# Optimization experiments

Measured on AMD Instinct MI355X. Metric: run time of the kernel, lower is better.

## Reference

```python
import jax, jax.numpy as jnp
import numpy as np

B, S, D = 8, 2048, 768
SCALE = jnp.sqrt(jnp.float32(D))


def setup_inputs() -> dict:
    key = jax.random.key(0)
    ks = jax.random.split(key, 9)
    sd = 1.0 / np.sqrt(D)
    return {
        "x": jax.random.normal(ks[0], (B, S, D), jnp.float32),
        "Wq": jax.random.normal(ks[1], (D, D), jnp.float32) * sd,
        "bq": jax.random.normal(ks[2], (D,), jnp.float32) * sd,
        "Wk": jax.random.normal(ks[3], (D, D), jnp.float32) * sd,
        "bk": jax.random.normal(ks[4], (D,), jnp.float32) * sd,
        "Wv": jax.random.normal(ks[5], (D, D), jnp.float32) * sd,
        "bv": jax.random.normal(ks[6], (D,), jnp.float32) * sd,
        "Wp": jax.random.normal(ks[7], (D, D), jnp.float32) * sd,
        "bp": jax.random.normal(ks[8], (D,), jnp.float32) * sd,
    }


def reference(x, Wq, bq, Wk, bk, Wv, bv, Wp, bp):
    # Linear layers: y = x @ W^T + b (torch nn.Linear convention)
    Q = jnp.einsum("bsd,ed->bse", x, Wq) + bq
    K = jnp.einsum("bsd,ed->bse", x, Wk) + bk
    V = jnp.einsum("bsd,ed->bse", x, Wv) + bv
    # Full attention matrix (no head split in original module)
    alpha = jnp.einsum("bqd,bkd->bqk", Q, K) / SCALE  # [B,S,S]
    alpha = jax.nn.softmax(alpha, axis=-1)
    # dropout is identity in eval mode
    out = jnp.einsum("bqk,bkd->bqd", alpha, V)
    out = jnp.einsum("bsd,ed->bse", out, Wp) + bp
    return out
```

## Files before the change

### kernel.cpp

```cpp
#include <hip/hip_runtime.h>
#include <stdint.h>


typedef __attribute__((ext_vector_type(8))) short short8;
typedef __attribute__((ext_vector_type(4))) float f32x4;

typedef const __attribute__((address_space(1))) void gvoid_t;
typedef __attribute__((address_space(3))) void lvoid_t;

__device__ __forceinline__ float b2f(unsigned short u) {
  union { unsigned int u; float f; } v;
  v.u = ((unsigned int)u) << 16;
  return v.f;
}
__device__ __forceinline__ unsigned short f2b(float f) {
  union { float f; unsigned int u; } v; v.f = f;
  unsigned int u = v.u;
  return (unsigned short)((u + 0x7fffu + ((u >> 16) & 1u)) >> 16);
}

struct Cvt9 {
  const void* s[9];
  unsigned short* d[9];
  long long n8[9];
  long long total8;
};

__global__ __launch_bounds__(256) void convert_inputs(Cvt9 C) {
  long long g = (long long)blockIdx.x * 256 + threadIdx.x;
  if (g >= C.total8) return;
  int s = 0;
  long long off = g;
  while (off >= C.n8[s]) { off -= C.n8[s]; ++s; }
  const float* sf = (const float*)C.s[s] + off * 8;
  unsigned short* dp = C.d[s] + off * 8;
  float4 a = ((const float4*)sf)[0];
  float4 b = ((const float4*)sf)[1];
  uint4 o;
  o.x = (unsigned int)f2b(a.x) | ((unsigned int)f2b(a.y) << 16);
  o.y = (unsigned int)f2b(a.z) | ((unsigned int)f2b(a.w) << 16);
  o.z = (unsigned int)f2b(b.x) | ((unsigned int)f2b(b.y) << 16);
  o.w = (unsigned int)f2b(b.z) | ((unsigned int)f2b(b.w) << 16);
  *(uint4*)dp = o;
}

__device__ __forceinline__ void gemm256(
    const unsigned short* __restrict__ Ag,
    const unsigned short* __restrict__ Bg,
    const int lda, const int ldb, const int NT,
    unsigned short* lds, f32x4 (&acc)[8][4])
{
  const int t    = threadIdx.x;
  const int w    = t >> 6;
  const int lane = t & 63;
  const int lo   = lane & 15;
  const int quad = lane >> 4;
  const int wr   = w >> 2;
  const int wcn  = w & 3;
  const int swz  = ((t & 7) ^ ((t >> 3) & 7)) << 3;
  const int wslot = w * 512;

  const unsigned lbase = (unsigned)(uintptr_t)(void*)lds;
  const unsigned sb0 = (unsigned)((quad ^ (lo & 7)) << 4);
  const unsigned sb1 = (unsigned)(((4 + quad) ^ (lo & 7)) << 4);
  const unsigned aA0 = lbase + wr * 16384 + lo * 128 + sb0;
  const unsigned aA1 = lbase + wr * 16384 + lo * 128 + sb1;
  const unsigned aB0 = lbase + 32768 + (wcn >> 1) * 16384 + ((wcn & 1) * 64 + lo) * 128 + sb0;
  const unsigned aB1 = lbase + 32768 + (wcn >> 1) * 16384 + ((wcn & 1) * 64 + lo) * 128 + sb1;

  short8 af[4][2], bf0[2][2], bf1[2][2];

#define STG(gb, ld, kt, q, reg)                                                   \
  __builtin_amdgcn_global_load_lds(                                               \
      (gvoid_t*)((gb) + (size_t)((q) * 64 + (t >> 3)) * (ld) + (kt) * 64 + swz),  \
      (lvoid_t*)((reg) + wslot), 16, 0, 0)
#define SA02(kt) { unsigned short* r_ = lds + ((kt) & 1) * 32768;         \
                   STG(Ag, lda, (kt), 0, r_); STG(Ag, lda, (kt), 2, r_ + 8192); }
#define SA13(kt) { unsigned short* r_ = lds + ((kt) & 1) * 32768;         \
                   STG(Ag, lda, (kt), 1, r_ + 4096); STG(Ag, lda, (kt), 3, r_ + 12288); }
#define SB01(kt) { unsigned short* r_ = lds + ((kt) & 1) * 32768 + 16384; \
                   STG(Bg, ldb, (kt), 0, r_); STG(Bg, ldb, (kt), 1, r_ + 4096); }
#define SB23(kt) { unsigned short* r_ = lds + ((kt) & 1) * 32768 + 16384; \
                   STG(Bg, ldb, (kt), 2, r_ + 8192); STG(Bg, ldb, (kt), 3, r_ + 12288); }
#define DSR(d, a, IMM) asm volatile("ds_read_b128 %0, %1 offset:" #IMM : "=v"(d) : "v"(a))
#define RDA(MH, bo) {                                                 \
  const unsigned a0_ = aA0 + (bo) + (MH) * 8192;                      \
  const unsigned a1_ = aA1 + (bo) + (MH) * 8192;                      \
  DSR(af[0][0], a0_, 0);    DSR(af[0][1], a1_, 0);                    \
  DSR(af[1][0], a0_, 2048); DSR(af[1][1], a1_, 2048);                 \
  DSR(af[2][0], a0_, 4096); DSR(af[2][1], a1_, 4096);                 \
  DSR(af[3][0], a0_, 6144); DSR(af[3][1], a1_, 6144); }
#define RDB(BF, NH, bo) {                                             \
  const unsigned b0_ = aB0 + (bo) + (NH) * 4096;                      \
  const unsigned b1_ = aB1 + (bo) + (NH) * 4096;                      \
  DSR(BF[0][0], b0_, 0);    DSR(BF[0][1], b1_, 0);                    \
  DSR(BF[1][0], b0_, 2048); DSR(BF[1][1], b1_, 2048); }
#define MMA(MH, NH, BF) {                                                     \
  __builtin_amdgcn_s_barrier();                                               \
  asm volatile("s_waitcnt lgkmcnt(0)" ::: "memory");                          \
  __builtin_amdgcn_sched_barrier(0);                                          \
  __builtin_amdgcn_s_setprio(1);                                              \
  _Pragma("unroll") for (int kc = 0; kc < 2; ++kc)                            \
  _Pragma("unroll") for (int mi = 0; mi < 4; ++mi)                            \
  _Pragma("unroll") for (int ni = 0; ni < 2; ++ni)                            \
    acc[(MH)*4 + mi][(NH)*2 + ni] = __builtin_amdgcn_mfma_f32_16x16x32_bf16(  \
        af[mi][kc], BF[ni][kc], acc[(MH)*4 + mi][(NH)*2 + ni], 0, 0, 0);      \
  __builtin_amdgcn_s_setprio(0);                                              \
  __builtin_amdgcn_sched_barrier(0);                                          \
  __builtin_amdgcn_s_barrier(); }
#define VM(n) asm volatile("s_waitcnt vmcnt(" #n ")" ::: "memory")

  SA02(0); SB01(0); SB23(0); SA13(0);
  SA02(1); SB01(1); SB23(1); SA13(1);
  VM(8);
  __builtin_amdgcn_s_barrier();

  for (int kt = 0; kt < NT - 2; ++kt) {
    const unsigned bo = (unsigned)(kt & 1) << 16;
    RDA(0, bo); RDB(bf0, 0, bo);                          MMA(0, 0, bf0);
    RDB(bf1, 1, bo); SA02(kt + 2);                        MMA(0, 1, bf1);
    RDA(1, bo); SB01(kt + 2); SB23(kt + 2);               MMA(1, 0, bf0);
    SA13(kt + 2); VM(8);                                  MMA(1, 1, bf1);
  }
  {
    const unsigned bo = (unsigned)(NT & 1) << 16;
    RDA(0, bo); RDB(bf0, 0, bo);                          MMA(0, 0, bf0);
    RDB(bf1, 1, bo);                                      MMA(0, 1, bf1);
    RDA(1, bo);                                           MMA(1, 0, bf0);
    VM(0);                                                MMA(1, 1, bf1);
  }
  {
    const unsigned bo = (unsigned)((NT - 1) & 1) << 16;
    RDA(0, bo); RDB(bf0, 0, bo);                          MMA(0, 0, bf0);
    RDB(bf1, 1, bo);                                      MMA(0, 1, bf1);
    RDA(1, bo);                                           MMA(1, 0, bf0);
                                                          MMA(1, 1, bf1);
  }
#undef STG
#undef SA02
#undef SA13
#undef SB01
#undef SB23
#undef DSR
#undef RDA
#undef RDB
#undef MMA
#undef VM
}

template<int MODE>
__device__ __forceinline__ void epi_bf16(
    unsigned short* Ls, f32x4 (&acc)[8][4], int h,
    const unsigned short* bias_n0, const float* rlbase, float scale,
    unsigned short* Cg, int ldc)
{
  const int t = threadIdx.x, w = t >> 6, lane = t & 63;
  const int lo = lane & 15, quad = lane >> 4, wr = w >> 2, wcn = w & 3;
  __syncthreads();
  if (wr == h) {
    float bvv[4];
    if (MODE == 0) {
#pragma unroll
      for (int nf = 0; nf < 4; ++nf) bvv[nf] = b2f(bias_n0[wcn * 64 + nf * 16 + lo]);
    }
#pragma unroll
    for (int mf = 0; mf < 8; ++mf) {
      const int r0 = mf * 16 + quad * 4;
      float rv[4];
      if (MODE == 3) {
#pragma unroll
        for (int r = 0; r < 4; ++r) rv[r] = __builtin_amdgcn_rcpf(rlbase[h * 128 + r0 + r]);
      }
#pragma unroll
      for (int nf = 0; nf < 4; ++nf) {
        const int col = wcn * 64 + nf * 16 + lo;
#pragma unroll
        for (int r = 0; r < 4; ++r) {
          float v = acc[mf][nf][r];
          if (MODE == 0)      v += bvv[nf];
          else if (MODE == 2) v = __expf(fminf(v * scale, 30.f));
          else if (MODE == 3) v *= rv[r];
          Ls[(r0 + r) * 264 + col] = f2b(v);
        }
      }
    }
  }
  __syncthreads();
#pragma unroll
  for (int u0 = 0; u0 < 8; ++u0) {
    const int u = u0 * 512 + t, row = u >> 5, c16 = (u & 31) * 8;
    *(uint4*)(Cg + (size_t)(h * 128 + row) * ldc + c16) = *(const uint4*)(Ls + row * 264 + c16);
  }
}

__global__ __launch_bounds__(512, 2) void qkv_k(
    const unsigned short* __restrict__ xb,
    const unsigned short* __restrict__ Wq, const unsigned short* __restrict__ bq,
    const unsigned short* __restrict__ Wk, const unsigned short* __restrict__ bk,
    const unsigned short* __restrict__ Wv, const unsigned short* __restrict__ bv,
    unsigned short* __restrict__ qb, unsigned short* __restrict__ kb,
    unsigned short* __restrict__ vt)
{
  __shared__ unsigned short smem[65536];
  const int sel = blockIdx.y / 3;
  const int n0  = (blockIdx.y % 3) * 256;
  const int m0  = blockIdx.x * 256;

  const unsigned short* W;
  const unsigned short* bi;
  if (sel == 0)      { W = Wq; bi = bq; }
  else if (sel == 1) { W = Wk; bi = bk; }
  else               { W = Wv; bi = bv; }

  f32x4 acc[8][4] = {};
  gemm256(xb + (size_t)m0 * 768, W + (size_t)n0 * 768, 768, 768, 12, smem, acc);

  if (sel < 2) {
    unsigned short* dst = (sel == 0 ? qb : kb) + (size_t)m0 * 768 + n0;
    epi_bf16<0>(smem, acc, 0, bi + n0, nullptr, 0.f, dst, 768);
    epi_bf16<0>(smem, acc, 1, bi + n0, nullptr, 0.f, dst, 768);
    return;
  }

  const int t = threadIdx.x, w = t >> 6, lane = t & 63;
  const int lo = lane & 15, quad = lane >> 4, wr = w >> 2, wcn = w & 3;
  const int bb2 = m0 >> 11, sin = m0 & 2047;
  unsigned short* Ls = smem;
#pragma unroll
  for (int eh = 0; eh < 2; ++eh) {
    __syncthreads();
    if ((wcn >> 1) == eh) {
#pragma unroll
      for (int mf = 0; mf < 8; ++mf) {
        const int row = wr * 128 + mf * 16 + quad * 4;
#pragma unroll
        for (int nf = 0; nf < 4; ++nf) {
          const int colL = (wcn & 1) * 64 + nf * 16 + lo;
          const float bvv = b2f(bi[n0 + eh * 128 + colL]);
          ushort4 pk;
          pk.x = f2b(acc[mf][nf][0] + bvv);
          pk.y = f2b(acc[mf][nf][1] + bvv);
          pk.z = f2b(acc[mf][nf][2] + bvv);
          pk.w = f2b(acc[mf][nf][3] + bvv);
          *(ushort4*)(Ls + colL * 264 + row) = pk;
        }
      }
    }
    __syncthreads();
    unsigned short* Vb = vt + (size_t)bb2 * 1572864 + (size_t)(n0 + eh * 128) * 2048 + sin;
#pragma unroll
    for (int u0 = 0; u0 < 8; ++u0) {
      const int u = u0 * 512 + t, e = u >> 5, s16 = (u & 31) * 8;
      *(uint4*)(Vb + (size_t)e * 2048 + s16) = *(const uint4*)(Ls + e * 264 + s16);
    }
  }
}

__global__ __launch_bounds__(512, 2) void score_k(
    const unsigned short* __restrict__ Q, const unsigned short* __restrict__ Kb,
    unsigned short* __restrict__ E, float* __restrict__ rl, float scale)
{
  __shared__ unsigned short smem[65536];
  const int m0 = blockIdx.x * 256, n0 = blockIdx.y * 256, bz = blockIdx.z;

  f32x4 acc[8][4] = {};
  gemm256(Q + (size_t)bz * 1572864 + (size_t)m0 * 768,
          Kb + (size_t)bz * 1572864 + (size_t)n0 * 768, 768, 768, 12, smem, acc);

  const int t = threadIdx.x;
  unsigned short* Eg = E + (size_t)bz * 4194304 + (size_t)m0 * 2048 + n0;
#pragma unroll
  for (int h = 0; h < 2; ++h) {
    epi_bf16<2>(smem, acc, h, nullptr, nullptr, scale, Eg, 2048);
    const int row = t >> 2, seg = t & 3;
    const unsigned short* lr = smem + row * 264 + seg * 64;
    float s = 0.f;
#pragma unroll
    for (int q8 = 0; q8 < 8; ++q8) {
      const int qq = ((q8 + row) & 7) * 8;
      uint4 v = *(const uint4*)(lr + qq);
      unsigned int uu[4] = {v.x, v.y, v.z, v.w};
#pragma unroll
      for (int c = 0; c < 4; ++c)
        s += b2f((unsigned short)(uu[c] & 0xffffu)) + b2f((unsigned short)(uu[c] >> 16));
    }
    s += __shfl_xor(s, 1);
    s += __shfl_xor(s, 2);
    if (seg == 0) atomicAdd(rl + bz * 2048 + m0 + h * 128 + row, s);
  }
}

__global__ __launch_bounds__(512, 2) void pv_k(
    const unsigned short* __restrict__ E, const unsigned short* __restrict__ Vt,
    const float* __restrict__ rl, unsigned short* __restrict__ attn)
{
  __shared__ unsigned short smem[65536];
  const int m0 = blockIdx.x * 256, n0 = blockIdx.y * 256, bz = blockIdx.z;

  f32x4 acc[8][4] = {};
  gemm256(E + (size_t)bz * 4194304 + (size_t)m0 * 2048,
          Vt + (size_t)bz * 1572864 + (size_t)n0 * 2048, 2048, 2048, 32, smem, acc);

  const float* rlb = rl + bz * 2048 + m0;
  unsigned short* Cg = attn + (size_t)bz * 1572864 + (size_t)m0 * 768 + n0;
  epi_bf16<3>(smem, acc, 0, nullptr, rlb, 0.f, Cg, 768);
  epi_bf16<3>(smem, acc, 1, nullptr, rlb, 0.f, Cg, 768);
}

__global__ __launch_bounds__(512, 2) void out_k(
    const unsigned short* __restrict__ attn,
    const unsigned short* __restrict__ Wp, const unsigned short* __restrict__ bp,
    float* __restrict__ Of)
{
  __shared__ unsigned short smem[65536];
  const int m0 = blockIdx.x * 256, n0 = blockIdx.y * 256;

  f32x4 acc[8][4] = {};
  gemm256(attn + (size_t)m0 * 768, Wp + (size_t)n0 * 768, 768, 768, 12, smem, acc);

  const int t = threadIdx.x, w = t >> 6, lane = t & 63;
  const int lo = lane & 15, quad = lane >> 4, wr = w >> 2, wcn = w & 3;
  float* Lf = (float*)smem;
#pragma unroll
  for (int p = 0; p < 4; ++p) {
    __syncthreads();
    if (wr == (p >> 1)) {
#pragma unroll
      for (int mi = 0; mi < 4; ++mi) {
        const int mf = (p & 1) * 4 + mi;
        const int r0 = mi * 16 + quad * 4;
#pragma unroll
        for (int nf = 0; nf < 4; ++nf) {
          const int col = wcn * 64 + nf * 16 + lo;
          const float bvv = b2f(bp[n0 + col]);
#pragma unroll
          for (int r = 0; r < 4; ++r)
            Lf[(r0 + r) * 264 + col] = acc[mf][nf][r] + bvv;
        }
      }
    }
    __syncthreads();
#pragma unroll
    for (int u0 = 0; u0 < 8; ++u0) {
      const int u = u0 * 512 + t, row = u >> 6, c4 = (u & 63) * 4;
      *(float4*)(Of + (size_t)(m0 + p * 64 + row) * 768 + n0 + c4) =
          *(const float4*)(Lf + row * 264 + c4);
    }
  }
}

extern "C" void kernel_launch(void* const* d_in, const int* in_sizes, int n_in,
                              void* d_out, int out_size, void* d_ws, size_t ws_size,
                              hipStream_t stream) {
  (void)in_sizes; (void)n_in; (void)out_size; (void)ws_size;

  char* ws = (char*)d_ws;
  float* rl    = (float*)(ws + 4096);
  unsigned short* wcv = (unsigned short*)(ws + ((size_t)1 << 20));
  unsigned short* qb  = (unsigned short*)(ws + ((size_t)8  << 20));
  unsigned short* kb  = (unsigned short*)(ws + ((size_t)32 << 20));
  unsigned short* vt  = (unsigned short*)(ws + ((size_t)56 << 20));
  unsigned short* eb  = (unsigned short*)(ws + ((size_t)80 << 20));
  unsigned short* xb  = eb;
  unsigned short* attn = qb;

  unsigned short* wqb = wcv;
  unsigned short* bqb = wcv + 589824;
  unsigned short* wkb = wcv + 590592;
  unsigned short* bkb = wcv + 1180416;
  unsigned short* wvb = wcv + 1181184;
  unsigned short* bvb = wcv + 1771008;
  unsigned short* wpb = wcv + 1771776;
  unsigned short* bpb = wcv + 2361600;

  const float inv_scale = 0.036084391824351615f;

  Cvt9 cv;
  cv.s[0] = d_in[0]; cv.d[0] = xb;  cv.n8[0] = 12582912 / 8;
  cv.s[1] = d_in[1]; cv.d[1] = wqb; cv.n8[1] = 589824 / 8;
  cv.s[2] = d_in[2]; cv.d[2] = bqb; cv.n8[2] = 768 / 8;
  cv.s[3] = d_in[3]; cv.d[3] = wkb; cv.n8[3] = 589824 / 8;
  cv.s[4] = d_in[4]; cv.d[4] = bkb; cv.n8[4] = 768 / 8;
  cv.s[5] = d_in[5]; cv.d[5] = wvb; cv.n8[5] = 589824 / 8;
  cv.s[6] = d_in[6]; cv.d[6] = bvb; cv.n8[6] = 768 / 8;
  cv.s[7] = d_in[7]; cv.d[7] = wpb; cv.n8[7] = 589824 / 8;
  cv.s[8] = d_in[8]; cv.d[8] = bpb; cv.n8[8] = 768 / 8;
  cv.total8 = (12582912 + 4 * (589824 + 768)) / 8;
  convert_inputs<<<(unsigned)((cv.total8 + 255) / 256), dim3(256), 0, stream>>>(cv);

  hipMemsetAsync(rl, 0, 16384 * sizeof(float), stream);

  qkv_k<<<dim3(64, 9, 1), dim3(512), 0, stream>>>(xb, wqb, bqb, wkb, bkb, wvb, bvb, qb, kb, vt);

  score_k<<<dim3(8, 8, 8), dim3(512), 0, stream>>>(qb, kb, eb, rl, inv_scale);

  pv_k<<<dim3(8, 3, 8), dim3(512), 0, stream>>>(eb, vt, rl, attn);

  out_k<<<dim3(64, 3, 1), dim3(512), 0, stream>>>(attn, wpb, bpb, (float*)d_out);
}
```

Before: 353.8 us.

## Use 256x192 GEMM tiles for the N=768 kernels to improve CU occupancy

Templates the 256x256 bf16 MFMA GEMM core on the number of N fragments per wave, so the qkv, pv and out kernels can use 256x192 tiles while score_k keeps 256x256. With N=768 split into four tiles instead of three, the grids grow (e.g. pv from 192 to 256 blocks), which is meant to fill the MI355X CUs better and reduce tail imbalance. LDS footprint, B staging, wait counts and epilogues are adjusted for the narrower tile. The cost is lower per-tile arithmetic intensity and more A-tile reloads.

```diff
diff --git a/kernel.cpp b/kernel.cpp
--- a/kernel.cpp
+++ b/kernel.cpp
@@ -44,11 +44,12 @@
   *(uint4*)dp = o;
 }
 
+template<int NQ>
 __device__ __forceinline__ void gemm256(
     const unsigned short* __restrict__ Ag,
     const unsigned short* __restrict__ Bg,
     const int lda, const int ldb, const int NT,
-    unsigned short* lds, f32x4 (&acc)[8][4])
+    unsigned short* lds, f32x4 (&acc)[8][NQ])
 {
   const int t    = threadIdx.x;
   const int w    = t >> 6;
@@ -59,14 +60,17 @@
   const int wcn  = w & 3;
   const int swz  = ((t & 7) ^ ((t >> 3) & 7)) << 3;
   const int wslot = w * 512;
+  constexpr int SBUF_B = (4 + NQ) * 8192;
+  constexpr int SBUF_S = SBUF_B / 2;
 
   const unsigned lbase = (unsigned)(uintptr_t)(void*)lds;
   const unsigned sb0 = (unsigned)((quad ^ (lo & 7)) << 4);
   const unsigned sb1 = (unsigned)(((4 + quad) ^ (lo & 7)) << 4);
   const unsigned aA0 = lbase + wr * 16384 + lo * 128 + sb0;
   const unsigned aA1 = lbase + wr * 16384 + lo * 128 + sb1;
-  const unsigned aB0 = lbase + 32768 + (wcn >> 1) * 16384 + ((wcn & 1) * 64 + lo) * 128 + sb0;
-  const unsigned aB1 = lbase + 32768 + (wcn >> 1) * 16384 + ((wcn & 1) * 64 + lo) * 128 + sb1;
+  const unsigned bB  = lbase + 32768u + (unsigned)(wcn * 16 * NQ + lo) * 128;
+  const unsigned aB0 = bB + sb0;
+  const unsigned aB1 = bB + sb1;
 
   short8 af[4][2], bf0[2][2], bf1[2][2];
 
@@ -74,14 +78,14 @@
   __builtin_amdgcn_global_load_lds(                                               \
       (gvoid_t*)((gb) + (size_t)((q) * 64 + (t >> 3)) * (ld) + (kt) * 64 + swz),  \
       (lvoid_t*)((reg) + wslot), 16, 0, 0)
-#define SA02(kt) { unsigned short* r_ = lds + ((kt) & 1) * 32768;         \
+#define SA02(kt) { unsigned short* r_ = lds + ((kt) & 1) * SBUF_S;         \
                    STG(Ag, lda, (kt), 0, r_); STG(Ag, lda, (kt), 2, r_ + 8192); }
-#define SA13(kt) { unsigned short* r_ = lds + ((kt) & 1) * 32768;         \
+#define SA13(kt) { unsigned short* r_ = lds + ((kt) & 1) * SBUF_S;         \
                    STG(Ag, lda, (kt), 1, r_ + 4096); STG(Ag, lda, (kt), 3, r_ + 12288); }
-#define SB01(kt) { unsigned short* r_ = lds + ((kt) & 1) * 32768 + 16384; \
-                   STG(Bg, ldb, (kt), 0, r_); STG(Bg, ldb, (kt), 1, r_ + 4096); }
-#define SB23(kt) { unsigned short* r_ = lds + ((kt) & 1) * 32768 + 16384; \
-                   STG(Bg, ldb, (kt), 2, r_ + 8192); STG(Bg, ldb, (kt), 3, r_ + 12288); }
+#define SBALL(kt) { unsigned short* r_ = lds + ((kt) & 1) * SBUF_S + 16384; \
+                    STG(Bg, ldb, (kt), 0, r_); STG(Bg, ldb, (kt), 1, r_ + 4096); \
+                    STG(Bg, ldb, (kt), 2, r_ + 8192); \
+                    if constexpr (NQ == 4) STG(Bg, ldb, (kt), 3, r_ + 12288); }
 #define DSR(d, a, IMM) asm volatile("ds_read_b128 %0, %1 offset:" #IMM : "=v"(d) : "v"(a))
 #define RDA(MH, bo) {                                                 \
   const unsigned a0_ = aA0 + (bo) + (MH) * 8192;                      \
@@ -90,78 +94,81 @@
   DSR(af[1][0], a0_, 2048); DSR(af[1][1], a1_, 2048);                 \
   DSR(af[2][0], a0_, 4096); DSR(af[2][1], a1_, 4096);                 \
   DSR(af[3][0], a0_, 6144); DSR(af[3][1], a1_, 6144); }
-#define RDB(BF, NH, bo) {                                             \
-  const unsigned b0_ = aB0 + (bo) + (NH) * 4096;                      \
-  const unsigned b1_ = aB1 + (bo) + (NH) * 4096;                      \
+#define RDB(BF, NB, NFR, bo) {                                        \
+  const unsigned b0_ = aB0 + (bo) + (NB) * 2048;                      \
+  const unsigned b1_ = aB1 + (bo) + (NB) * 2048;                      \
   DSR(BF[0][0], b0_, 0);    DSR(BF[0][1], b1_, 0);                    \
-  DSR(BF[1][0], b0_, 2048); DSR(BF[1][1], b1_, 2048); }
-#define MMA(MH, NH, BF) {                                                     \
+  if ((NFR) == 2) { DSR(BF[1][0], b0_, 2048); DSR(BF[1][1], b1_, 2048); } }
+#define MMA(MH, NB, BF, NFR) {                                                \
   __builtin_amdgcn_s_barrier();                                               \
   asm volatile("s_waitcnt lgkmcnt(0)" ::: "memory");                          \
   __builtin_amdgcn_sched_barrier(0);                                          \
   __builtin_amdgcn_s_setprio(1);                                              \
   _Pragma("unroll") for (int kc = 0; kc < 2; ++kc)                            \
   _Pragma("unroll") for (int mi = 0; mi < 4; ++mi)                            \
-  _Pragma("unroll") for (int ni = 0; ni < 2; ++ni)                            \
-    acc[(MH)*4 + mi][(NH)*2 + ni] = __builtin_amdgcn_mfma_f32_16x16x32_bf16(  \
-        af[mi][kc], BF[ni][kc], acc[(MH)*4 + mi][(NH)*2 + ni], 0, 0, 0);      \
+  _Pragma("unroll") for (int ni = 0; ni < (NFR); ++ni)                        \
+    acc[(MH)*4 + mi][(NB) + ni] = __builtin_amdgcn_mfma_f32_16x16x32_bf16(    \
+        af[mi][kc], BF[ni][kc], acc[(MH)*4 + mi][(NB) + ni], 0, 0, 0);        \
   __builtin_amdgcn_s_setprio(0);                                              \
   __builtin_amdgcn_sched_barrier(0);                                          \
   __builtin_amdgcn_s_barrier(); }
-#define VM(n) asm volatile("s_waitcnt vmcnt(" #n ")" ::: "memory")
-
-  SA02(0); SB01(0); SB23(0); SA13(0);
-  SA02(1); SB01(1); SB23(1); SA13(1);
-  VM(8);
+#define VMS() { if constexpr (NQ == 4) asm volatile("s_waitcnt vmcnt(8)" ::: "memory"); \
+                else                   asm volatile("s_waitcnt vmcnt(7)" ::: "memory"); }
+#define VM0() asm volatile("s_waitcnt vmcnt(0)" ::: "memory")
+
+  SA02(0); SBALL(0); SA13(0);
+  SA02(1); SBALL(1); SA13(1);
+  VMS();
   __builtin_amdgcn_s_barrier();
 
   for (int kt = 0; kt < NT - 2; ++kt) {
-    const unsigned bo = (unsigned)(kt & 1) << 16;
-    RDA(0, bo); RDB(bf0, 0, bo);                          MMA(0, 0, bf0);
-    RDB(bf1, 1, bo); SA02(kt + 2);                        MMA(0, 1, bf1);
-    RDA(1, bo); SB01(kt + 2); SB23(kt + 2);               MMA(1, 0, bf0);
-    SA13(kt + 2); VM(8);                                  MMA(1, 1, bf1);
+    const unsigned bo = (unsigned)((kt & 1) * SBUF_B);
+    RDA(0, bo); RDB(bf0, 0, 2, bo);                       MMA(0, 0, bf0, 2);
+    RDB(bf1, 2, NQ - 2, bo); SA02(kt + 2);                MMA(0, 2, bf1, NQ - 2);
+    RDA(1, bo); SBALL(kt + 2);                            MMA(1, 0, bf0, 2);
+    SA13(kt + 2); VMS();                                  MMA(1, 2, bf1, NQ - 2);
   }
   {
-    const unsigned bo = (unsigned)(NT & 1) << 16;
-    RDA(0, bo); RDB(bf0, 0, bo);                          MMA(0, 0, bf0);
-    RDB(bf1, 1, bo);                                      MMA(0, 1, bf1);
-    RDA(1, bo);                                           MMA(1, 0, bf0);
-    VM(0);                                                MMA(1, 1, bf1);
+    const unsigned bo = (unsigned)((NT & 1) * SBUF_B);
+    RDA(0, bo); RDB(bf0, 0, 2, bo);                       MMA(0, 0, bf0, 2);
+    RDB(bf1, 2, NQ - 2, bo);                              MMA(0, 2, bf1, NQ - 2);
+    RDA(1, bo);                                           MMA(1, 0, bf0, 2);
+    VM0();                                                MMA(1, 2, bf1, NQ - 2);
   }
   {
-    const unsigned bo = (unsigned)((NT - 1) & 1) << 16;
-    RDA(0, bo); RDB(bf0, 0, bo);                          MMA(0, 0, bf0);
-    RDB(bf1, 1, bo);                                      MMA(0, 1, bf1);
-    RDA(1, bo);                                           MMA(1, 0, bf0);
-                                                          MMA(1, 1, bf1);
+    const unsigned bo = (unsigned)(((NT - 1) & 1) * SBUF_B);
+    RDA(0, bo); RDB(bf0, 0, 2, bo);                       MMA(0, 0, bf0, 2);
+    RDB(bf1, 2, NQ - 2, bo);                              MMA(0, 2, bf1, NQ - 2);
+    RDA(1, bo);                                           MMA(1, 0, bf0, 2);
+                                                          MMA(1, 2, bf1, NQ - 2);
   }
 #undef STG
 #undef SA02
 #undef SA13
-#undef SB01
-#undef SB23
+#undef SBALL
 #undef DSR
 #undef RDA
 #undef RDB
 #undef MMA
-#undef VM
-}
-
-template<int MODE>
+#undef VMS
+#undef VM0
+}
+
+template<int MODE, int NQ>
 __device__ __forceinline__ void epi_bf16(
-    unsigned short* Ls, f32x4 (&acc)[8][4], int h,
+    unsigned short* Ls, f32x4 (&acc)[8][NQ], int h,
     const unsigned short* bias_n0, const float* rlbase, float scale,
     unsigned short* Cg, int ldc)
 {
+  constexpr int RS = 64 * NQ + 8;
   const int t = threadIdx.x, w = t >> 6, lane = t & 63;
   const int lo = lane & 15, quad = lane >> 4, wr = w >> 2, wcn = w & 3;
   __syncthreads();
   if (wr == h) {
-    float bvv[4];
+    float bvv[NQ];
     if (MODE == 0) {
 #pragma unroll
-      for (int nf = 0; nf < 4; ++nf) bvv[nf] = b2f(bias_n0[wcn * 64 + nf * 16 + lo]);
+      for (int nf = 0; nf < NQ; ++nf) bvv[nf] = b2f(bias_n0[wcn * 16 * NQ + nf * 16 + lo]);
     }
 #pragma unroll
     for (int mf = 0; mf < 8; ++mf) {
@@ -172,24 +179,24 @@
         for (int r = 0; r < 4; ++r) rv[r] = __builtin_amdgcn_rcpf(rlbase[h * 128 + r0 + r]);
       }
 #pragma unroll
-      for (int nf = 0; nf < 4; ++nf) {
-        const int col = wcn * 64 + nf * 16 + lo;
+      for (int nf = 0; nf < NQ; ++nf) {
+        const int col = wcn * 16 * NQ + nf * 16 + lo;
 #pragma unroll
         for (int r = 0; r < 4; ++r) {
           float v = acc[mf][nf][r];
           if (MODE == 0)      v += bvv[nf];
           else if (MODE == 2) v = __expf(fminf(v * scale, 30.f));
           else if (MODE == 3) v *= rv[r];
-          Ls[(r0 + r) * 264 + col] = f2b(v);
+          Ls[(r0 + r) * RS + col] = f2b(v);
         }
       }
     }
   }
   __syncthreads();
 #pragma unroll
-  for (int u0 = 0; u0 < 8; ++u0) {
-    const int u = u0 * 512 + t, row = u >> 5, c16 = (u & 31) * 8;
-    *(uint4*)(Cg + (size_t)(h * 128 + row) * ldc + c16) = *(const uint4*)(Ls + row * 264 + c16);
+  for (int u0 = 0; u0 < 2 * NQ; ++u0) {
+    const int u = u0 * 512 + t, row = u / (8 * NQ), c16 = (u % (8 * NQ)) * 8;
+    *(uint4*)(Cg + (size_t)(h * 128 + row) * ldc + c16) = *(const uint4*)(Ls + row * RS + c16);
   }
 }
 
@@ -201,9 +208,9 @@
     unsigned short* __restrict__ qb, unsigned short* __restrict__ kb,
     unsigned short* __restrict__ vt)
 {
-  __shared__ unsigned short smem[65536];
-  const int sel = blockIdx.y / 3;
-  const int n0  = (blockIdx.y % 3) * 256;
+  __shared__ unsigned short smem[57344];
+  const int sel = blockIdx.y >> 2;
+  const int n0  = (blockIdx.y & 3) * 192;
   const int m0  = blockIdx.x * 256;
 
   const unsigned short* W;
@@ -212,13 +219,13 @@
   else if (sel == 1) { W = Wk; bi = bk; }
   else               { W = Wv; bi = bv; }
 
-  f32x4 acc[8][4] = {};
-  gemm256(xb + (size_t)m0 * 768, W + (size_t)n0 * 768, 768, 768, 12, smem, acc);
+  f32x4 acc[8][3] = {};
+  gemm256<3>(xb + (size_t)m0 * 768, W + (size_t)n0 * 768, 768, 768, 12, smem, acc);
 
   if (sel < 2) {
     unsigned short* dst = (sel == 0 ? qb : kb) + (size_t)m0 * 768 + n0;
-    epi_bf16<0>(smem, acc, 0, bi + n0, nullptr, 0.f, dst, 768);
-    epi_bf16<0>(smem, acc, 1, bi + n0, nullptr, 0.f, dst, 768);
+    epi_bf16<0, 3>(smem, acc, 0, bi + n0, nullptr, 0.f, dst, 768);
+    epi_bf16<0, 3>(smem, acc, 1, bi + n0, nullptr, 0.f, dst, 768);
     return;
   }
 
@@ -227,29 +234,29 @@
   const int bb2 = m0 >> 11, sin = m0 & 2047;
   unsigned short* Ls = smem;
 #pragma unroll
-  for (int eh = 0; eh < 2; ++eh) {
+  for (int ec = 0; ec < 3; ++ec) {
     __syncthreads();
-    if ((wcn >> 1) == eh) {
-#pragma unroll
-      for (int mf = 0; mf < 8; ++mf) {
-        const int row = wr * 128 + mf * 16 + quad * 4;
-#pragma unroll
-        for (int nf = 0; nf < 4; ++nf) {
-          const int colL = (wcn & 1) * 64 + nf * 16 + lo;
-          const float bvv = b2f(bi[n0 + eh * 128 + colL]);
+#pragma unroll
+    for (int nf = 0; nf < 3; ++nf) {
+      const int ebase = wcn * 48 + nf * 16;
+      if ((ebase >> 6) == ec) {
+        const float bvv = b2f(bi[n0 + ebase + lo]);
+#pragma unroll
+        for (int mf = 0; mf < 8; ++mf) {
+          const int srow = wr * 128 + mf * 16 + quad * 4;
           ushort4 pk;
           pk.x = f2b(acc[mf][nf][0] + bvv);
           pk.y = f2b(acc[mf][nf][1] + bvv);
           pk.z = f2b(acc[mf][nf][2] + bvv);
           pk.w = f2b(acc[mf][nf][3] + bvv);
-          *(ushort4*)(Ls + colL * 264 + row) = pk;
+          *(ushort4*)(Ls + ((ebase & 63) + lo) * 264 + srow) = pk;
         }
       }
     }
     __syncthreads();
-    unsigned short* Vb = vt + (size_t)bb2 * 1572864 + (size_t)(n0 + eh * 128) * 2048 + sin;
-#pragma unroll
-    for (int u0 = 0; u0 < 8; ++u0) {
+    unsigned short* Vb = vt + (size_t)bb2 * 1572864 + (size_t)(n0 + ec * 64) * 2048 + sin;
+#pragma unroll
+    for (int u0 = 0; u0 < 4; ++u0) {
       const int u = u0 * 512 + t, e = u >> 5, s16 = (u & 31) * 8;
       *(uint4*)(Vb + (size_t)e * 2048 + s16) = *(const uint4*)(Ls + e * 264 + s16);
     }
@@ -264,14 +271,14 @@
   const int m0 = blockIdx.x * 256, n0 = blockIdx.y * 256, bz = blockIdx.z;
 
   f32x4 acc[8][4] = {};
-  gemm256(Q + (size_t)bz * 1572864 + (size_t)m0 * 768,
-          Kb + (size_t)bz * 1572864 + (size_t)n0 * 768, 768, 768, 12, smem, acc);
+  gemm256<4>(Q + (size_t)bz * 1572864 + (size_t)m0 * 768,
+             Kb + (size_t)bz * 1572864 + (size_t)n0 * 768, 768, 768, 12, smem, acc);
 
   const int t = threadIdx.x;
   unsigned short* Eg = E + (size_t)bz * 4194304 + (size_t)m0 * 2048 + n0;
 #pragma unroll
   for (int h = 0; h < 2; ++h) {
-    epi_bf16<2>(smem, acc, h, nullptr, nullptr, scale, Eg, 2048);
+    epi_bf16<2, 4>(smem, acc, h, nullptr, nullptr, scale, Eg, 2048);
     const int row = t >> 2, seg = t & 3;
     const unsigned short* lr = smem + row * 264 + seg * 64;
     float s = 0.f;
@@ -294,17 +301,17 @@
     const unsigned short* __restrict__ E, const unsigned short* __restrict__ Vt,
     const float* __restrict__ rl, unsigned short* __restrict__ attn)
 {
-  __shared__ unsigned short smem[65536];
-  const int m0 = blockIdx.x * 256, n0 = blockIdx.y * 256, bz = blockIdx.z;
-
-  f32x4 acc[8][4] = {};
-  gemm256(E + (size_t)bz * 4194304 + (size_t)m0 * 2048,
-          Vt + (size_t)bz * 1572864 + (size_t)n0 * 2048, 2048, 2048, 32, smem, acc);
+  __shared__ unsigned short smem[57344];
+  const int m0 = blockIdx.x * 256, n0 = blockIdx.y * 192, bz = blockIdx.z;
+
+  f32x4 acc[8][3] = {};
+  gemm256<3>(E + (size_t)bz * 4194304 + (size_t)m0 * 2048,
+             Vt + (size_t)bz * 1572864 + (size_t)n0 * 2048, 2048, 2048, 32, smem, acc);
 
   const float* rlb = rl + bz * 2048 + m0;
   unsigned short* Cg = attn + (size_t)bz * 1572864 + (size_t)m0 * 768 + n0;
-  epi_bf16<3>(smem, acc, 0, nullptr, rlb, 0.f, Cg, 768);
-  epi_bf16<3>(smem, acc, 1, nullptr, rlb, 0.f, Cg, 768);
+  epi_bf16<3, 3>(smem, acc, 0, nullptr, rlb, 0.f, Cg, 768);
+  epi_bf16<3, 3>(smem, acc, 1, nullptr, rlb, 0.f, Cg, 768);
 }
 
 __global__ __launch_bounds__(512, 2) void out_k(
@@ -312,11 +319,11 @@
     const unsigned short* __restrict__ Wp, const unsigned short* __restrict__ bp,
     float* __restrict__ Of)
 {
-  __shared__ unsigned short smem[65536];
-  const int m0 = blockIdx.x * 256, n0 = blockIdx.y * 256;
-
-  f32x4 acc[8][4] = {};
-  gemm256(attn + (size_t)m0 * 768, Wp + (size_t)n0 * 768, 768, 768, 12, smem, acc);
+  __shared__ unsigned short smem[57344];
+  const int m0 = blockIdx.x * 256, n0 = blockIdx.y * 192;
+
+  f32x4 acc[8][3] = {};
+  gemm256<3>(attn + (size_t)m0 * 768, Wp + (size_t)n0 * 768, 768, 768, 12, smem, acc);
 
   const int t = threadIdx.x, w = t >> 6, lane = t & 63;
   const int lo = lane & 15, quad = lane >> 4, wr = w >> 2, wcn = w & 3;
@@ -330,21 +337,21 @@
         const int mf = (p & 1) * 4 + mi;
         const int r0 = mi * 16 + quad * 4;
 #pragma unroll
-        for (int nf = 0; nf < 4; ++nf) {
-          const int col = wcn * 64 + nf * 16 + lo;
+        for (int nf = 0; nf < 3; ++nf) {
+          const int col = wcn * 48 + nf * 16 + lo;
           const float bvv = b2f(bp[n0 + col]);
 #pragma unroll
           for (int r = 0; r < 4; ++r)
-            Lf[(r0 + r) * 264 + col] = acc[mf][nf][r] + bvv;
+            Lf[(r0 + r) * 196 + col] = acc[mf][nf][r] + bvv;
         }
       }
     }
     __syncthreads();
 #pragma unroll
-    for (int u0 = 0; u0 < 8; ++u0) {
-      const int u = u0 * 512 + t, row = u >> 6, c4 = (u & 63) * 4;
+    for (int u0 = 0; u0 < 6; ++u0) {
+      const int u = u0 * 512 + t, row = u / 48, c4 = (u % 48) * 4;
       *(float4*)(Of + (size_t)(m0 + p * 64 + row) * 768 + n0 + c4) =
-          *(const float4*)(Lf + row * 264 + c4);
+          *(const float4*)(Lf + row * 196 + c4);
     }
   }
 }
@@ -390,11 +397,11 @@
 
   hipMemsetAsync(rl, 0, 16384 * sizeof(float), stream);
 
-  qkv_k<<<dim3(64, 9, 1), dim3(512), 0, stream>>>(xb, wqb, bqb, wkb, bkb, wvb, bvb, qb, kb, vt);
+  qkv_k<<<dim3(64, 12, 1), dim3(512), 0, stream>>>(xb, wqb, bqb, wkb, bkb, wvb, bvb, qb, kb, vt);
 
   score_k<<<dim3(8, 8, 8), dim3(512), 0, stream>>>(qb, kb, eb, rl, inv_scale);
 
-  pv_k<<<dim3(8, 3, 8), dim3(512), 0, stream>>>(eb, vt, rl, attn);
-
-  out_k<<<dim3(64, 3, 1), dim3(512), 0, stream>>>(attn, wpb, bpb, (float*)d_out);
-}
+  pv_k<<<dim3(8, 4, 8), dim3(512), 0, stream>>>(eb, vt, rl, attn);
+
+  out_k<<<dim3(64, 4, 1), dim3(512), 0, stream>>>(attn, wpb, bpb, (float*)d_out);
+}
```

Result: faster. 321.0 us (-9.3%).
